# Optimization experiments

Measured on AMD Instinct MI355X. Metric: run time of the kernel, lower is better.

## Reference

```python
import jax, jax.numpy as jnp
import numpy as np

T, H, NH, NKV, HD = 4096, 2048, 16, 2, 256
ROT = 64           # partial_rotary_factor 0.25 * head_dim 256
HALF = ROT // 2    # 32 == sum(mrope_section [11, 11, 10])
BASE = 10_000_000.0
EPS = 1e-6
SCALE = HD ** -0.5


def setup_inputs() -> dict:
    key = jax.random.key(0)
    ks = jax.random.split(key, 8)
    s = 0.02
    return {
        "positions": jnp.sort(jax.random.randint(ks[0], (3, T), 0, 4096), axis=-1),
        "hidden": jax.random.normal(ks[1], (T, H), jnp.float32),
        "Wq": jax.random.normal(ks[2], (H, NH * HD * 2), jnp.float32) * s,
        "Wk": jax.random.normal(ks[3], (H, NKV * HD), jnp.float32) * s,
        "Wv": jax.random.normal(ks[4], (H, NKV * HD), jnp.float32) * s,
        "Wo": jax.random.normal(ks[5], (NH * HD, H), jnp.float32) * s,
        "q_norm_w": jax.random.normal(ks[6], (HD,), jnp.float32) * 0.1,
        "k_norm_w": jax.random.normal(ks[7], (HD,), jnp.float32) * 0.1,
    }


def _rms(x, w):
    # GemmaRMSNorm: x / rms * (1 + w), per-head over last dim
    var = jnp.mean(x * x, axis=-1, keepdims=True)
    return x * jax.lax.rsqrt(var + EPS) * (1.0 + w)


def _rope_tables(positions):
    # interleaved MRoPE: freq j uses position axis j % 3 -> counts [11,11,10]
    inv_freq = BASE ** (-jnp.arange(0, ROT, 2, dtype=jnp.float32) / ROT)  # [HALF]
    axis = jnp.arange(HALF) % 3
    pos = positions[axis, :].astype(jnp.float32)   # [HALF, T]
    freqs = pos.T * inv_freq                       # [T, HALF]
    return jnp.cos(freqs), jnp.sin(freqs)


def _apply_rope(x, cos, sin):
    # x: [T, heads, HD]; rotate first ROT dims (neox half-split), rest pass through
    x1, x2 = x[..., :HALF], x[..., HALF:ROT]
    c, s = cos[:, None, :], sin[:, None, :]
    return jnp.concatenate([x1 * c - x2 * s, x2 * c + x1 * s, x[..., ROT:]], axis=-1)


def reference(positions, hidden, Wq, Wk, Wv, Wo, q_norm_w, k_norm_w):
    qg = (hidden @ Wq).reshape(T, NH, 2 * HD)
    q, gate = qg[..., :HD], qg[..., HD:]          # chunk(2, dim=-1)
    k = (hidden @ Wk).reshape(T, NKV, HD)
    v = (hidden @ Wv).reshape(T, NKV, HD)
    q = _rms(q, q_norm_w)
    k = _rms(k, k_norm_w)
    cos, sin = _rope_tables(positions)
    q = _apply_rope(q, cos, sin)
    k = _apply_rope(k, cos, sin)
    # GQA causal attention: group 16 Q heads over 2 KV heads
    g = NH // NKV
    q4 = q.reshape(T, NKV, g, HD)
    scores = jnp.einsum('qkgd,tkd->kgqt', q4, k) * SCALE   # [NKV, g, T, T]
    mask = jnp.tril(jnp.ones((T, T), dtype=bool))
    scores = jnp.where(mask[None, None], scores, -jnp.inf)
    probs = jax.nn.softmax(scores, axis=-1)
    o = jnp.einsum('kgqt,tkd->qkgd', probs, v).reshape(T, NH, HD)
    o = o * jax.nn.sigmoid(gate)                   # per-head output gating
    return o.reshape(T, NH * HD) @ Wo
```

## Files before the change

kernel.cpp:

```cpp
#include <hip/hip_runtime.h>
#include <hip/hip_bf16.h>


#define T_SZ 4096
#define H_SZ 2048
#define NH_SZ 16
#define NKV_SZ 2
#define HD_SZ 256
#define ATT_SCALE 0.0625f
#define SOFT_M 18.0f
#define EPS_ 1e-6f

typedef __attribute__((ext_vector_type(8))) short bf16x8;
typedef __attribute__((ext_vector_type(4))) float f32x4;

#define MFMA16(a, b, c) __builtin_amdgcn_mfma_f32_16x16x32_bf16((a), (b), (c), 0, 0, 0)

__device__ __forceinline__ void async16(const void* g, void* l) {
  __builtin_amdgcn_global_load_lds((const __attribute__((address_space(1))) void*)g,
                                   (__attribute__((address_space(3))) void*)l,
                                   16, 0, 0);
}

__device__ __forceinline__ float to_f(float x) { return x; }
__device__ __forceinline__ float to_f(__hip_bfloat16 x) { return __bfloat162float(x); }

union BfBits { __hip_bfloat16 h; unsigned short u; };

__device__ __forceinline__ unsigned short bf16_bits(__hip_bfloat16 h) {
  BfBits t; t.h = h; return t.u;
}

__device__ __forceinline__ unsigned pack_hilo(float v) {
  __hip_bfloat16 hi = __float2bfloat16(v);
  float rem = v - __bfloat162float(hi);
  __hip_bfloat16 lo = __float2bfloat16(rem);
  return (unsigned)bf16_bits(hi) | ((unsigned)bf16_bits(lo) << 16);
}

__global__ __launch_bounds__(256) void cast_f32_bf16(const float* __restrict__ in,
                                                     __hip_bfloat16* __restrict__ out,
                                                     int n4) {
  int i = blockIdx.x * 256 + threadIdx.x;
  if (i >= n4) return;
  float4 v = ((const float4*)in)[i];
  union { __hip_bfloat16 h[4]; uint2 u; } t;
  t.h[0] = __float2bfloat16(v.x);
  t.h[1] = __float2bfloat16(v.y);
  t.h[2] = __float2bfloat16(v.z);
  t.h[3] = __float2bfloat16(v.w);
  ((uint2*)out)[i] = t.u;
}

template <typename TIN>
__global__ __launch_bounds__(256) void transpose_cast(const TIN* __restrict__ in,
                                                      __hip_bfloat16* __restrict__ out,
                                                      int R, int C) {
  __shared__ TIN tile[32][33];
  int c0 = blockIdx.x * 32, r0 = blockIdx.y * 32;
  int tx = threadIdx.x & 31, ty = threadIdx.x >> 5;
#pragma unroll
  for (int i = 0; i < 32; i += 8)
    tile[ty + i][tx] = in[(long)(r0 + ty + i) * C + c0 + tx];
  __syncthreads();
#pragma unroll
  for (int i = 0; i < 32; i += 8)
    out[(long)(c0 + ty + i) * R + r0 + tx] = __float2bfloat16(to_f(tile[tx][ty + i]));
}

__global__ __launch_bounds__(256) void gemm_qg(const __hip_bfloat16* __restrict__ A,
                                               const __hip_bfloat16* __restrict__ BT,
                                               float* __restrict__ qout,
                                               __hip_bfloat16* __restrict__ gate,
                                               int M, int N, int K) {
  __shared__ __align__(16) __hip_bfloat16 As[128 * 32];
  __shared__ __align__(16) __hip_bfloat16 Bs[128 * 32];
  const int tid = threadIdx.x;
  const int wid = tid >> 6, lane = tid & 63;
  const int lo = lane & 15, quad = lane >> 4;
  const int wq = blockIdx.x + blockIdx.y * 64;
  const int xcd = wq & 7, idx = wq >> 3;
  const long n0 = (long)(xcd * 8 + (idx & 7)) * 128;
  const long m0 = (long)(idx >> 3) * 128;
  const int wm = (wid >> 1) * 64, wn = (wid & 1) * 64;
  const f32x4 z4 = {0.f, 0.f, 0.f, 0.f};
  f32x4 acc[4][4];
#pragma unroll
  for (int i = 0; i < 4; ++i)
#pragma unroll
    for (int j = 0; j < 4; ++j) acc[i][j] = z4;

  const int cf0 = tid, cf1 = 256 + tid;
  const int r0_ = cf0 >> 2, c0_ = (cf0 & 3) * 8;
  const int r1_ = cf1 >> 2, c1_ = (cf1 & 3) * 8;
  const __hip_bfloat16* a0 = A + (m0 + r0_) * K + c0_;
  const __hip_bfloat16* a1 = A + (m0 + r1_) * K + c1_;
  const __hip_bfloat16* b0 = BT + (n0 + r0_) * K + c0_;
  const __hip_bfloat16* b1 = BT + (n0 + r1_) * K + c1_;

  for (int k0 = 0; k0 < K; k0 += 32) {
    async16(a0 + k0, As + cf0 * 8);
    async16(a1 + k0, As + cf1 * 8);
    async16(b0 + k0, Bs + cf0 * 8);
    async16(b1 + k0, Bs + cf1 * 8);
    __syncthreads();
    bf16x8 af[4], bfv[4];
#pragma unroll
    for (int i = 0; i < 4; ++i)
      af[i] = *(const bf16x8*)(As + (wm + i * 16 + lo) * 32 + quad * 8);
#pragma unroll
    for (int i = 0; i < 4; ++i)
      bfv[i] = *(const bf16x8*)(Bs + (wn + i * 16 + lo) * 32 + quad * 8);
#pragma unroll
    for (int i = 0; i < 4; ++i)
#pragma unroll
      for (int j = 0; j < 4; ++j) acc[i][j] = MFMA16(af[i], bfv[j], acc[i][j]);
    __syncthreads();
  }
#pragma unroll
  for (int i = 0; i < 4; ++i)
#pragma unroll
    for (int j = 0; j < 4; ++j)
#pragma unroll
      for (int r = 0; r < 4; ++r) {
        long row = m0 + wm + i * 16 + quad * 4 + r;
        long col = n0 + wn + j * 16 + lo;
        int head = (int)(col >> 9), c = (int)(col & 511);
        float v = acc[i][j][r];
        if (c < 256)
          qout[(row * NH_SZ + head) * 256 + c] = v;
        else
          gate[(row * NH_SZ + head) * 256 + (c - 256)] = __float2bfloat16(v);
      }
}

__global__ __launch_bounds__(256) void gemm_kv(const __hip_bfloat16* __restrict__ A,
                                               const __hip_bfloat16* __restrict__ BT,
                                               float* __restrict__ kf,
                                               __hip_bfloat16* __restrict__ vraw,
                                               int M, int N, int K) {
  __shared__ __align__(16) __hip_bfloat16 As[128 * 32];
  __shared__ __align__(16) __hip_bfloat16 Bs[128 * 32];
  const int tid = threadIdx.x;
  const int wid = tid >> 6, lane = tid & 63;
  const int lo = lane & 15, quad = lane >> 4;
  const int wq = blockIdx.x + blockIdx.y * 8;
  const int xcd = wq & 7, idx = wq >> 3;
  const long n0 = (long)xcd * 128;
  const long m0 = (long)idx * 128;
  const int wm = (wid >> 1) * 64, wn = (wid & 1) * 64;
  const f32x4 z4 = {0.f, 0.f, 0.f, 0.f};
  f32x4 acc[4][4];
#pragma unroll
  for (int i = 0; i < 4; ++i)
#pragma unroll
    for (int j = 0; j < 4; ++j) acc[i][j] = z4;

  const int cf0 = tid, cf1 = 256 + tid;
  const int r0_ = cf0 >> 2, c0_ = (cf0 & 3) * 8;
  const int r1_ = cf1 >> 2, c1_ = (cf1 & 3) * 8;
  const __hip_bfloat16* a0 = A + (m0 + r0_) * K + c0_;
  const __hip_bfloat16* a1 = A + (m0 + r1_) * K + c1_;
  const __hip_bfloat16* b0 = BT + (n0 + r0_) * K + c0_;
  const __hip_bfloat16* b1 = BT + (n0 + r1_) * K + c1_;

  for (int k0 = 0; k0 < K; k0 += 32) {
    async16(a0 + k0, As + cf0 * 8);
    async16(a1 + k0, As + cf1 * 8);
    async16(b0 + k0, Bs + cf0 * 8);
    async16(b1 + k0, Bs + cf1 * 8);
    __syncthreads();
    bf16x8 af[4], bfv[4];
#pragma unroll
    for (int i = 0; i < 4; ++i)
      af[i] = *(const bf16x8*)(As + (wm + i * 16 + lo) * 32 + quad * 8);
#pragma unroll
    for (int i = 0; i < 4; ++i)
      bfv[i] = *(const bf16x8*)(Bs + (wn + i * 16 + lo) * 32 + quad * 8);
#pragma unroll
    for (int i = 0; i < 4; ++i)
#pragma unroll
      for (int j = 0; j < 4; ++j) acc[i][j] = MFMA16(af[i], bfv[j], acc[i][j]);
    __syncthreads();
  }
#pragma unroll
  for (int i = 0; i < 4; ++i)
#pragma unroll
    for (int j = 0; j < 4; ++j)
#pragma unroll
      for (int r = 0; r < 4; ++r) {
        long row = m0 + wm + i * 16 + quad * 4 + r;
        long col = n0 + wn + j * 16 + lo;
        float v = acc[i][j][r];
        if (col < 512)
          kf[row * 512 + col] = v;
        else
          vraw[row * 512 + (col - 512)] = __float2bfloat16(v);
      }
}

__global__ __launch_bounds__(256) void v_swizzle(const __hip_bfloat16* __restrict__ vraw,
                                                 __hip_bfloat16* __restrict__ vsw) {
  const int ktt = blockIdx.x, kvh = blockIdx.y, tid = threadIdx.x;
  __shared__ __hip_bfloat16 L[64 * 264];
#pragma unroll
  for (int it = 0; it < 8; ++it) {
    int cf = it * 256 + tid;
    int kv = cf >> 5, d0 = (cf & 31) * 8;
    *(uint4*)&L[kv * 264 + d0] =
        *(const uint4*)&vraw[(((long)ktt * 64 + kv) * NKV_SZ + kvh) * 256 + d0];
  }
  __syncthreads();
#pragma unroll
  for (int it = 0; it < 8; ++it) {
    int cf = it * 256 + tid;
    int c = cf >> 8, d = cf & 255;
    union { __hip_bfloat16 h[8]; uint4 u; } t;
#pragma unroll
    for (int e = 0; e < 8; ++e) t.h[e] = L[(c * 8 + e) * 264 + d];
    *(uint4*)&vsw[((long)kvh * 64 + ktt) * 16384 + (long)(c * 256 + d) * 8] = t.u;
  }
}

__global__ __launch_bounds__(256) void norm_rope_wave(float* __restrict__ qbuf,
                                                      const float* __restrict__ kbuf,
                                                      __hip_bfloat16* __restrict__ ksw,
                                                      const int* __restrict__ pos,
                                                      const float* __restrict__ qw,
                                                      const float* __restrict__ kw) {
  const int id = blockIdx.x * 4 + (threadIdx.x >> 6);
  const int lane = threadIdx.x & 63;
  const int h = id % 18, t = id / 18;
  const bool isq = h < NH_SZ;
  const float* ptr = isq ? qbuf + ((long)t * NH_SZ + h) * 256
                         : kbuf + ((long)t * NKV_SZ + (h - NH_SZ)) * 256;
  const float* w = isq ? qw : kw;
  float4 v = *(const float4*)(ptr + lane * 4);
  float4 wv = *(const float4*)(w + lane * 4);
  float s2 = v.x * v.x + v.y * v.y + v.z * v.z + v.w * v.w;
#pragma unroll
  for (int o = 32; o > 0; o >>= 1) s2 += __shfl_xor(s2, o);
  float sc = rsqrtf(s2 * (1.0f / 256.0f) + EPS_);
  float n[4];
  n[0] = v.x * sc * (1.0f + wv.x);
  n[1] = v.y * sc * (1.0f + wv.y);
  n[2] = v.z * sc * (1.0f + wv.z);
  n[3] = v.w * sc * (1.0f + wv.w);
  float pr[4];
#pragma unroll
  for (int j = 0; j < 4; ++j) pr[j] = __shfl_xor(n[j], 8);
  float o4[4];
  if (lane < 16) {
    int base_i = (lane & 7) * 4;
#pragma unroll
    for (int j = 0; j < 4; ++j) {
      int i = base_i + j;
      float p = (float)pos[(i % 3) * T_SZ + t];
      float fr = p * exp2f((float)i * (-0.72667177075661f));
      float c, s;
      sincosf(fr, &s, &c);
      o4[j] = (lane < 8) ? n[j] * c - pr[j] * s : n[j] * c + pr[j] * s;
    }
  } else {
#pragma unroll
    for (int j = 0; j < 4; ++j) o4[j] = n[j];
  }
  if (isq) {
    uint4 u;
    u.x = pack_hilo(o4[0]); u.y = pack_hilo(o4[1]);
    u.z = pack_hilo(o4[2]); u.w = pack_hilo(o4[3]);
    *(uint4*)((unsigned*)qbuf + ((long)t * NH_SZ + h) * 256 + lane * 4) = u;
  } else {
    int kv = h - NH_SZ;
    long tt = t >> 5; int r = t & 31;
    int c = lane >> 1, e0 = (lane & 1) * 4;
    union { __hip_bfloat16 h4[4]; uint2 u; } kk;
#pragma unroll
    for (int j = 0; j < 4; ++j) kk.h4[j] = __float2bfloat16(o4[j]);
    *(uint2*)&ksw[(((long)kv * 128 + tt) * 32 + c) * 256 + r * 8 + e0] = kk.u;
  }
}

__global__ __launch_bounds__(256) void attn_kernel(unsigned* __restrict__ Qp,
                                                   const __hip_bfloat16* __restrict__ Ksw,
                                                   const __hip_bfloat16* __restrict__ Vsw,
                                                   const __hip_bfloat16* __restrict__ Gt) {
  const int w = blockIdx.x + blockIdx.y * 64;
  const int xcd = w & 7, j = w >> 3;
  const int h = xcd * 2 + (j & 1);
  const int qt = 63 - (j >> 1);
  const int kvh = h >> 3;
  const int tid = threadIdx.x, wid = tid >> 6, lane = tid & 63;
  const int lo = lane & 15, quad = lane >> 4;
  __shared__ __align__(16) __hip_bfloat16 Ks[32 * 256];
  __shared__ __align__(16) __hip_bfloat16 Vs[4 * 2048];
  __shared__ __align__(16) __hip_bfloat16 Ps[4][16 * 40];

  __hip_bfloat16* myP = &Ps[wid][0];
  const f32x4 z4 = {0.f, 0.f, 0.f, 0.f};
  const int nt = 2 * (qt + 1);

  bf16x8 qh[8], ql[8];
  {
    const unsigned* qp =
        Qp + ((long)(qt * 64 + wid * 16 + lo) * NH_SZ + h) * 256 + quad * 8;
#pragma unroll
    for (int kc = 0; kc < 8; ++kc) {
      uint4 p0 = *(const uint4*)(qp + kc * 32);
      uint4 p1 = *(const uint4*)(qp + kc * 32 + 4);
      bf16x8 a, b;
      a[0] = (short)(p0.x & 0xffff); b[0] = (short)(p0.x >> 16);
      a[1] = (short)(p0.y & 0xffff); b[1] = (short)(p0.y >> 16);
      a[2] = (short)(p0.z & 0xffff); b[2] = (short)(p0.z >> 16);
      a[3] = (short)(p0.w & 0xffff); b[3] = (short)(p0.w >> 16);
      a[4] = (short)(p1.x & 0xffff); b[4] = (short)(p1.x >> 16);
      a[5] = (short)(p1.y & 0xffff); b[5] = (short)(p1.y >> 16);
      a[6] = (short)(p1.z & 0xffff); b[6] = (short)(p1.z >> 16);
      a[7] = (short)(p1.w & 0xffff); b[7] = (short)(p1.w >> 16);
      qh[kc] = a; ql[kc] = b;
    }
  }

  f32x4 acc[16];
#pragma unroll
  for (int od = 0; od < 16; ++od) acc[od] = z4;
  float lsum[4];
#pragma unroll
  for (int r = 0; r < 4; ++r) lsum[r] = 0.f;

  const int qrow_g = qt * 64 + wid * 16 + quad * 4;
  const __hip_bfloat16* kbase = Ksw + (long)kvh * 1048576;
  const __hip_bfloat16* vbase = Vsw + (long)kvh * 1048576;

#pragma unroll
  for (int i = 0; i < 4; ++i) {
    int m = i * 4 + wid;
    async16(kbase + m * 512 + lane * 8, Ks + m * 512 + lane * 8);
    async16(vbase + m * 512 + lane * 8, Vs + m * 512 + lane * 8);
  }
  __syncthreads();

  for (int kt = 0; kt < nt; ++kt) {
    const bool skip = (kt == nt - 1) && (wid < 2);
    f32x4 s[2];
    s[0] = z4; s[1] = z4;
    if (!skip) {
      __builtin_amdgcn_s_setprio(1);
#pragma unroll
      for (int kc = 0; kc < 8; ++kc) {
        bf16x8 ah = qh[kc], al = ql[kc];
#pragma unroll
        for (int ni = 0; ni < 2; ++ni) {
          bf16x8 b = *(const bf16x8*)(Ks + (kc * 4 + quad) * 256 + (ni * 16 + lo) * 8);
          s[ni] = MFMA16(ah, b, s[ni]);
          s[ni] = MFMA16(al, b, s[ni]);
        }
      }
      __builtin_amdgcn_s_setprio(0);
    }
    __syncthreads();
    if (kt + 1 < nt) {
      const __hip_bfloat16* kb = kbase + (long)(kt + 1) * 8192;
#pragma unroll
      for (int i = 0; i < 4; ++i) {
        int m = i * 4 + wid;
        async16(kb + m * 512 + lane * 8, Ks + m * 512 + lane * 8);
      }
    }
    if (!skip) {
      float sv[2][4];
      if (kt >= nt - 2) {
#pragma unroll
        for (int ni = 0; ni < 2; ++ni) {
          int kcol = kt * 32 + ni * 16 + lo;
#pragma unroll
          for (int r = 0; r < 4; ++r) {
            float e = __expf(fmaf(s[ni][r], ATT_SCALE, -SOFT_M));
            sv[ni][r] = (kcol > qrow_g + r) ? 0.f : e;
          }
        }
      } else {
#pragma unroll
        for (int ni = 0; ni < 2; ++ni)
#pragma unroll
          for (int r = 0; r < 4; ++r)
            sv[ni][r] = __expf(fmaf(s[ni][r], ATT_SCALE, -SOFT_M));
      }
#pragma unroll
      for (int r = 0; r < 4; ++r) lsum[r] += sv[0][r] + sv[1][r];
#pragma unroll
      for (int ni = 0; ni < 2; ++ni)
#pragma unroll
        for (int r = 0; r < 4; ++r)
          myP[(quad * 4 + r) * 40 + ni * 16 + lo] = __float2bfloat16(sv[ni][r]);
      bf16x8 ap = *(const bf16x8*)(myP + lo * 40 + quad * 8);
      __builtin_amdgcn_s_setprio(1);
#pragma unroll
      for (int od = 0; od < 16; ++od) {
        bf16x8 bv = *(const bf16x8*)(Vs + quad * 2048 + (od * 16 + lo) * 8);
        acc[od] = MFMA16(ap, bv, acc[od]);
      }
      __builtin_amdgcn_s_setprio(0);
    }
    __syncthreads();
    if (kt + 1 < nt) {
      const __hip_bfloat16* vb = vbase + (long)(kt + 1) * 8192;
#pragma unroll
      for (int i = 0; i < 4; ++i) {
        int m = i * 4 + wid;
        async16(vb + m * 512 + lane * 8, Vs + m * 512 + lane * 8);
      }
    }
  }

  float l_r[4];
#pragma unroll
  for (int r = 0; r < 4; ++r) {
    float su = lsum[r];
#pragma unroll
    for (int off = 1; off < 16; off <<= 1) su += __shfl_xor(su, off);
    l_r[r] = su;
  }
#pragma unroll
  for (int od = 0; od < 16; ++od)
#pragma unroll
    for (int r = 0; r < 4; ++r) {
      int trow = qt * 64 + wid * 16 + quad * 4 + r;
      int col = od * 16 + lo;
      long idx = ((long)trow * NH_SZ + h) * 256 + col;
      float g = __bfloat162float(Gt[idx]);
      float sig = 1.0f / (1.0f + expf(-g));
      float v = (acc[od][r] / l_r[r]) * sig;
      Qp[idx] = pack_hilo(v);
    }
}

__global__ __launch_bounds__(256) void gemm_out(const unsigned* __restrict__ Ap,
                                                const __hip_bfloat16* __restrict__ Bt,
                                                float* __restrict__ C,
                                                int M, int N, int K) {
  __shared__ __align__(16) __hip_bfloat16 Ash[128 * 32];
  __shared__ __align__(16) __hip_bfloat16 Asl[128 * 32];
  __shared__ __align__(16) __hip_bfloat16 Bs[128 * 32];
  const int tid = threadIdx.x;
  const int wid = tid >> 6, lane = tid & 63;
  const int lo = lane & 15, quad = lane >> 4;
  const int wq = blockIdx.x + blockIdx.y * 16;
  const int xcd = wq & 7, idx = wq >> 3;
  const long n0 = (long)(xcd * 2 + (idx & 1)) * 128;
  const long m0 = (long)(idx >> 1) * 128;
  const int wm = (wid >> 1) * 64, wn = (wid & 1) * 64;
  const f32x4 z4 = {0.f, 0.f, 0.f, 0.f};
  f32x4 acc[4][4];
#pragma unroll
  for (int i = 0; i < 4; ++i)
#pragma unroll
    for (int j = 0; j < 4; ++j) acc[i][j] = z4;

  const int cf0 = tid, cf1 = 256 + tid;
  const int br0 = cf0 >> 2, bc0 = (cf0 & 3) * 8;
  const int br1 = cf1 >> 2, bc1 = (cf1 & 3) * 8;
  const __hip_bfloat16* b0 = Bt + (n0 + br0) * K + bc0;
  const __hip_bfloat16* b1 = Bt + (n0 + br1) * K + bc1;

  for (int k0 = 0; k0 < K; k0 += 32) {
    async16(b0 + k0, Bs + cf0 * 8);
    async16(b1 + k0, Bs + cf1 * 8);
#pragma unroll
    for (int it = 0; it < 4; ++it) {
      int c = it * 256 + tid, row = c >> 3, c4 = (c & 7) * 4;
      uint4 p = *(const uint4*)(Ap + (m0 + row) * K + k0 + c4);
      uint2 wh, wl;
      wh.x = (p.x & 0xffff) | ((p.y & 0xffff) << 16);
      wh.y = (p.z & 0xffff) | ((p.w & 0xffff) << 16);
      wl.x = (p.x >> 16) | (p.y & 0xffff0000u);
      wl.y = (p.z >> 16) | (p.w & 0xffff0000u);
      *(uint2*)(Ash + row * 32 + c4) = wh;
      *(uint2*)(Asl + row * 32 + c4) = wl;
    }
    __syncthreads();
    bf16x8 ah[4], al[4], bf[4];
#pragma unroll
    for (int i = 0; i < 4; ++i) {
      ah[i] = *(const bf16x8*)(Ash + (wm + i * 16 + lo) * 32 + quad * 8);
      al[i] = *(const bf16x8*)(Asl + (wm + i * 16 + lo) * 32 + quad * 8);
      bf[i] = *(const bf16x8*)(Bs + (wn + i * 16 + lo) * 32 + quad * 8);
    }
#pragma unroll
    for (int i = 0; i < 4; ++i)
#pragma unroll
      for (int j = 0; j < 4; ++j) {
        acc[i][j] = MFMA16(ah[i], bf[j], acc[i][j]);
        acc[i][j] = MFMA16(al[i], bf[j], acc[i][j]);
      }
    __syncthreads();
  }
#pragma unroll
  for (int i = 0; i < 4; ++i)
#pragma unroll
    for (int j = 0; j < 4; ++j)
#pragma unroll
      for (int r = 0; r < 4; ++r) {
        long row = m0 + wm + i * 16 + quad * 4 + r;
        long col = n0 + wn + j * 16 + lo;
        C[row * N + col] = acc[i][j][r];
      }
}

extern "C" void kernel_launch(void* const* d_in, const int* in_sizes, int n_in,
                              void* d_out, int out_size, void* d_ws, size_t ws_size,
                              hipStream_t stream) {
  (void)in_sizes; (void)n_in; (void)out_size; (void)ws_size;
  const int* positions = (const int*)d_in[0];
  const float* hidden = (const float*)d_in[1];
  const float* Wq = (const float*)d_in[2];
  const float* Wk = (const float*)d_in[3];
  const float* Wv = (const float*)d_in[4];
  const float* Wo = (const float*)d_in[5];
  const float* qw = (const float*)d_in[6];
  const float* kw = (const float*)d_in[7];
  float* out = (float*)d_out;
  char* ws = (char*)d_ws;

  __hip_bfloat16* hid  = (__hip_bfloat16*)(ws + 0);
  __hip_bfloat16* WqT  = (__hip_bfloat16*)(ws + 16777216);
  __hip_bfloat16* WkT  = (__hip_bfloat16*)(ws + 50331648);
  __hip_bfloat16* WvT  = (__hip_bfloat16*)(ws + 52428800);
  float*          qf   = (float*)(ws + 54525952);
  __hip_bfloat16* gate = (__hip_bfloat16*)(ws + 121634816);
  float*          kf   = (float*)(ws + 155189248);
  __hip_bfloat16* vraw = (__hip_bfloat16*)(ws + 163577856);
  __hip_bfloat16* Ksw  = WkT;
  __hip_bfloat16* Vsw  = hid;
  __hip_bfloat16* WoT  = gate;
  unsigned* qpk = (unsigned*)qf;

  cast_f32_bf16<<<dim3(8192), dim3(256), 0, stream>>>(hidden, hid, 2097152);
  transpose_cast<float><<<dim3(256, 64), dim3(256), 0, stream>>>(Wq, WqT, 2048, 8192);
  transpose_cast<float><<<dim3(16, 64), dim3(256), 0, stream>>>(Wk, WkT, 2048, 512);
  transpose_cast<float><<<dim3(16, 64), dim3(256), 0, stream>>>(Wv, WvT, 2048, 512);
  gemm_qg<<<dim3(64, 32), dim3(256), 0, stream>>>(hid, WqT, qf, gate, 4096, 8192, 2048);
  gemm_kv<<<dim3(8, 32), dim3(256), 0, stream>>>(hid, WkT, kf, vraw, 4096, 1024, 2048);
  v_swizzle<<<dim3(64, 2), dim3(256), 0, stream>>>(vraw, Vsw);
  norm_rope_wave<<<dim3(18432), dim3(256), 0, stream>>>(qf, kf, Ksw, positions, qw, kw);
  attn_kernel<<<dim3(64, 16), dim3(256), 0, stream>>>(qpk, Ksw, Vsw, gate);
  transpose_cast<float><<<dim3(64, 128), dim3(256), 0, stream>>>(Wo, WoT, 4096, 2048);
  gemm_out<<<dim3(16, 32), dim3(256), 0, stream>>>(qpk, WoT, out, 4096, 2048, 4096);
}
```

Before: 903.5 us.

## Rewrite Q/gate GEMM with 256x256 tiles and 4-stage async LDS pipeline

Replaces the Q/gate projection GEMM with a 512-thread kernel that computes 256x256 output tiles. Global-to-LDS loads are issued asynchronously three k-steps ahead through a 4-buffer ring, with explicit vmcnt waits and a single barrier per iteration. LDS layout is XOR-swizzled to reduce bank conflicts, and MFMA issue gets raised wave priority. The larger tile raises operand reuse and hides load latency, at the cost of 64KB LDS and higher register pressure, which limits occupancy.

```diff
diff --git a/kernel.cpp b/kernel.cpp
--- a/kernel.cpp
+++ b/kernel.cpp
@@ -68,65 +68,98 @@
     out[(long)(c0 + ty + i) * R + r0 + tx] = __float2bfloat16(to_f(tile[tx][ty + i]));
 }
 
-__global__ __launch_bounds__(256) void gemm_qg(const __hip_bfloat16* __restrict__ A,
-                                               const __hip_bfloat16* __restrict__ BT,
-                                               float* __restrict__ qout,
-                                               __hip_bfloat16* __restrict__ gate,
-                                               int M, int N, int K) {
-  __shared__ __align__(16) __hip_bfloat16 As[128 * 32];
-  __shared__ __align__(16) __hip_bfloat16 Bs[128 * 32];
-  const int tid = threadIdx.x;
-  const int wid = tid >> 6, lane = tid & 63;
+__global__ __launch_bounds__(512) void gemm_qg2(const __hip_bfloat16* __restrict__ A,
+                                                const __hip_bfloat16* __restrict__ BT,
+                                                float* __restrict__ qout,
+                                                __hip_bfloat16* __restrict__ gate) {
+  __shared__ __align__(16) __hip_bfloat16 As[4][8192];
+  __shared__ __align__(16) __hip_bfloat16 Bs[4][8192];
+  const int tid = threadIdx.x, wid = tid >> 6, lane = tid & 63;
   const int lo = lane & 15, quad = lane >> 4;
-  const int wq = blockIdx.x + blockIdx.y * 64;
-  const int xcd = wq & 7, idx = wq >> 3;
-  const long n0 = (long)(xcd * 8 + (idx & 7)) * 128;
-  const long m0 = (long)(idx >> 3) * 128;
-  const int wm = (wid >> 1) * 64, wn = (wid & 1) * 64;
+  const int wm = (wid >> 2) * 128, wn = (wid & 3) * 64;
+  const int wg = blockIdx.x + blockIdx.y * 8;
+  const int xcd = wg & 7, i_ = wg >> 3;
+  const long n0 = (long)(xcd * 4 + (i_ & 3)) * 256;
+  const long m0 = (long)(i_ >> 2) * 256;
+  const int K = 2048;
+
+  const int r0_ = tid >> 2;
+  const int kc0 = (tid & 3) ^ ((tid >> 3) & 3);
+  const __hip_bfloat16* sA0 = A + (m0 + r0_) * K + kc0 * 8;
+  const __hip_bfloat16* sA1 = A + (m0 + r0_ + 128) * K + kc0 * 8;
+  const __hip_bfloat16* sB0 = BT + (n0 + r0_) * K + kc0 * 8;
+  const __hip_bfloat16* sB1 = BT + (n0 + r0_ + 128) * K + kc0 * 8;
+
+  const int xq = (lo >> 1) & 3;
+  const int aoff = (wm + lo) * 32 + ((quad ^ xq) * 8);
+  const int boff = (wn + lo) * 32 + ((quad ^ xq) * 8);
+
   const f32x4 z4 = {0.f, 0.f, 0.f, 0.f};
-  f32x4 acc[4][4];
-#pragma unroll
-  for (int i = 0; i < 4; ++i)
-#pragma unroll
-    for (int j = 0; j < 4; ++j) acc[i][j] = z4;
-
-  const int cf0 = tid, cf1 = 256 + tid;
-  const int r0_ = cf0 >> 2, c0_ = (cf0 & 3) * 8;
-  const int r1_ = cf1 >> 2, c1_ = (cf1 & 3) * 8;
-  const __hip_bfloat16* a0 = A + (m0 + r0_) * K + c0_;
-  const __hip_bfloat16* a1 = A + (m0 + r1_) * K + c1_;
-  const __hip_bfloat16* b0 = BT + (n0 + r0_) * K + c0_;
-  const __hip_bfloat16* b1 = BT + (n0 + r1_) * K + c1_;
-
-  for (int k0 = 0; k0 < K; k0 += 32) {
-    async16(a0 + k0, As + cf0 * 8);
-    async16(a1 + k0, As + cf1 * 8);
-    async16(b0 + k0, Bs + cf0 * 8);
-    async16(b1 + k0, Bs + cf1 * 8);
-    __syncthreads();
-    bf16x8 af[4], bfv[4];
-#pragma unroll
-    for (int i = 0; i < 4; ++i)
-      af[i] = *(const bf16x8*)(As + (wm + i * 16 + lo) * 32 + quad * 8);
-#pragma unroll
-    for (int i = 0; i < 4; ++i)
-      bfv[i] = *(const bf16x8*)(Bs + (wn + i * 16 + lo) * 32 + quad * 8);
-#pragma unroll
-    for (int i = 0; i < 4; ++i)
-#pragma unroll
-      for (int j = 0; j < 4; ++j) acc[i][j] = MFMA16(af[i], bfv[j], acc[i][j]);
-    __syncthreads();
-  }
-#pragma unroll
-  for (int i = 0; i < 4; ++i)
-#pragma unroll
-    for (int j = 0; j < 4; ++j)
-#pragma unroll
-      for (int r = 0; r < 4; ++r) {
-        long row = m0 + wm + i * 16 + quad * 4 + r;
-        long col = n0 + wn + j * 16 + lo;
+  f32x4 acc[8][4];
+#pragma unroll
+  for (int fr = 0; fr < 8; ++fr)
+#pragma unroll
+    for (int fn = 0; fn < 4; ++fn) acc[fr][fn] = z4;
+
+#define QG_STAGE(buf, kt) do {                                   \
+    const int off_ = (kt) * 32;                                  \
+    async16(sA0 + off_, &As[buf][tid * 8]);                      \
+    async16(sA1 + off_, &As[buf][tid * 8 + 4096]);               \
+    async16(sB0 + off_, &Bs[buf][tid * 8]);                      \
+    async16(sB1 + off_, &Bs[buf][tid * 8 + 4096]);               \
+  } while (0)
+
+#define QG_COMPUTE(buf_) do {                                    \
+    bf16x8 af[8], bq[4];                                         \
+    _Pragma("unroll")                                            \
+    for (int fr = 0; fr < 8; ++fr)                               \
+      af[fr] = *(const bf16x8*)(&As[buf_][aoff + fr * 512]);     \
+    _Pragma("unroll")                                            \
+    for (int fn = 0; fn < 4; ++fn)                               \
+      bq[fn] = *(const bf16x8*)(&Bs[buf_][boff + fn * 512]);     \
+    __builtin_amdgcn_s_setprio(1);                               \
+    _Pragma("unroll")                                            \
+    for (int fr = 0; fr < 8; ++fr)                               \
+      _Pragma("unroll")                                          \
+      for (int fn = 0; fn < 4; ++fn)                             \
+        acc[fr][fn] = MFMA16(af[fr], bq[fn], acc[fr][fn]);       \
+    __builtin_amdgcn_s_setprio(0);                               \
+  } while (0)
+
+  QG_STAGE(0, 0); QG_STAGE(1, 1); QG_STAGE(2, 2);
+  for (int kt = 0; kt < 61; ++kt) {
+    asm volatile("s_waitcnt vmcnt(8)" ::: "memory");
+    __builtin_amdgcn_s_barrier();
+    __builtin_amdgcn_sched_barrier(0);
+    QG_STAGE((kt + 3) & 3, kt + 3);
+    __builtin_amdgcn_sched_barrier(0);
+    QG_COMPUTE(kt & 3);
+  }
+  asm volatile("s_waitcnt vmcnt(8)" ::: "memory");
+  __builtin_amdgcn_s_barrier();
+  __builtin_amdgcn_sched_barrier(0);
+  QG_COMPUTE(1);
+  asm volatile("s_waitcnt vmcnt(4)" ::: "memory");
+  __builtin_amdgcn_s_barrier();
+  __builtin_amdgcn_sched_barrier(0);
+  QG_COMPUTE(2);
+  asm volatile("s_waitcnt vmcnt(0)" ::: "memory");
+  __builtin_amdgcn_s_barrier();
+  __builtin_amdgcn_sched_barrier(0);
+  QG_COMPUTE(3);
+#undef QG_STAGE
+#undef QG_COMPUTE
+
+#pragma unroll
+  for (int fr = 0; fr < 8; ++fr)
+#pragma unroll
+    for (int fn = 0; fn < 4; ++fn)
+#pragma unroll
+      for (int rr = 0; rr < 4; ++rr) {
+        long row = m0 + wm + fr * 16 + quad * 4 + rr;
+        long col = n0 + wn + fn * 16 + lo;
         int head = (int)(col >> 9), c = (int)(col & 511);
-        float v = acc[i][j][r];
+        float v = acc[fr][fn][rr];
         if (c < 256)
           qout[(row * NH_SZ + head) * 256 + c] = v;
         else
@@ -539,7 +572,7 @@
   transpose_cast<float><<<dim3(256, 64), dim3(256), 0, stream>>>(Wq, WqT, 2048, 8192);
   transpose_cast<float><<<dim3(16, 64), dim3(256), 0, stream>>>(Wk, WkT, 2048, 512);
   transpose_cast<float><<<dim3(16, 64), dim3(256), 0, stream>>>(Wv, WvT, 2048, 512);
-  gemm_qg<<<dim3(64, 32), dim3(256), 0, stream>>>(hid, WqT, qf, gate, 4096, 8192, 2048);
+  gemm_qg2<<<dim3(8, 64), dim3(512), 0, stream>>>(hid, WqT, qf, gate);
   gemm_kv<<<dim3(8, 32), dim3(256), 0, stream>>>(hid, WkT, kf, vraw, 4096, 1024, 2048);
   v_swizzle<<<dim3(64, 2), dim3(256), 0, stream>>>(vraw, Vsw);
   norm_rope_wave<<<dim3(18432), dim3(256), 0, stream>>>(qf, kf, Ksw, positions, qw, kw);
```

Measured after the change: 802.3 us. 1.13x faster.
